# Kernel optimization log

Hardware: AMD Instinct MI355X
Metric: run time of the kernel (lower is better)

The kernel has to match this reference:

```python
import jax, jax.numpy as jnp
import numpy as np
import math

EPS = 1e-07
ITERATIONS = 3
FINAL_LAMBDA = 0.01

B, H, W, K, CIN, COUT, P = 8, 12, 12, 3, 16, 32, 16


def setup_inputs() -> dict:
    key = jax.random.key(0)
    k1, k2, k3, k4 = jax.random.split(key, 4)
    V = jax.random.normal(k1, (B, H, W, K, K, CIN, COUT, P), dtype=jnp.float32)
    a = jax.random.uniform(k2, (B, H, W, K, K, CIN, 1), dtype=jnp.float32)
    Beta_u = jax.random.normal(k3, (1, 1, 1, 1, 1, 1, COUT, 1), dtype=jnp.float32)
    Beta_a = jax.random.normal(k4, (1, 1, 1, 1, 1, 1, COUT), dtype=jnp.float32)
    R = jnp.full((B, H, W, K, K, CIN, COUT), 1.0 / COUT, dtype=jnp.float32)
    outSize = (B, H, W, COUT, P)
    return {"V": V, "a": a, "Beta_u": Beta_u, "Beta_a": Beta_a, "R": R, "outSize": outSize}


def _l2_normalize(x, axis):
    n = jnp.sqrt(jnp.sum(x * x, axis=axis, keepdims=True))
    return x / jnp.maximum(n, 1e-12)  # matches F.normalize default eps


def reference(V, a, Beta_u, Beta_a, R, outSize):
    mathpilog = jnp.log(jnp.asarray(2.0 * math.pi, dtype=jnp.float32))
    mu = sigma_sqr = a_out = None
    for i in range(ITERATIONS):
        Lam = FINAL_LAMBDA * (1.0 - 0.95 ** (i + 1))
        Rw = (R * a)[..., None]                                  # [B,h,w,K,K,Cin,Cout,1]
        mu_denom = jnp.sum(Rw, axis=(3, 4, 5), keepdims=True)    # [B,h,w,1,1,1,Cout,1]
        mu = jnp.sum(Rw * V, axis=(3, 4, 5), keepdims=True) / (mu_denom + EPS)  # [B,h,w,1,1,1,Cout,P]
        V_mu_sqr = (V - mu) ** 2                                 # [B,h,w,K,K,Cin,Cout,P]
        sigma_sqr = jnp.sum(Rw * V_mu_sqr, axis=(3, 4, 5), keepdims=True) / (mu_denom + EPS)
        cost_h = (Beta_u + 0.5 * jnp.log(sigma_sqr)) * mu_denom  # [B,h,w,1,1,1,Cout,P]
        x = Lam * (Beta_a - jnp.sum(cost_h, axis=7))             # [B,h,w,1,1,1,Cout]
        a_out = jax.nn.sigmoid(_l2_normalize(x, axis=6))
        log_p1 = -0.5 * jnp.sum(mathpilog + jnp.log(sigma_sqr), axis=7) + EPS
        log_p2 = -jnp.sum(V_mu_sqr / (2.0 * sigma_sqr + EPS), axis=7)  # [B,h,w,K,K,Cin,Cout]
        R = jax.nn.softmax(jnp.log(a_out) + log_p1 + log_p2, axis=6)
    mu_out = jnp.squeeze(mu).reshape(outSize)
    sigma_out = jnp.squeeze(sigma_sqr).reshape(outSize)
    return mu_out, jnp.squeeze(a_out), sigma_out
```

## Files before the change

kernel.cpp:

```cpp
#include <hip/hip_runtime.h>
#include <math.h>

#define NPOS 1152
#define NN   144
#define COUT 32
#define PP   16
#define EPSF 1e-7f
#define LOG2PI 1.8378770664093453f

#define MU_OFF   0
#define A_OFF    589824
#define SIG_OFF  626688

template<int CTRL>
__device__ __forceinline__ float dppf(float x) {
    return __int_as_float(__builtin_amdgcn_update_dpp(
        0, __float_as_int(x), CTRL, 0xf, 0xf, true));
}

__device__ __forceinline__ float redmax32(float m) {
    m = fmaxf(m, dppf<0xB1>(m));
    m = fmaxf(m, dppf<0x4E>(m));
    m = fmaxf(m, dppf<0x141>(m));
    m = fmaxf(m, dppf<0x140>(m));
    m = fmaxf(m, __shfl_xor(m, 16, 64));
    return m;
}
__device__ __forceinline__ float redsum32(float s) {
    s += dppf<0xB1>(s);
    s += dppf<0x4E>(s);
    s += dppf<0x141>(s);
    s += dppf<0x140>(s);
    s += __shfl_xor(s, 16, 64);
    return s;
}

__global__ void __launch_bounds__(256, 4)
em_routing_kernel(const float* __restrict__ V,
                  const float* __restrict__ a,
                  const float* __restrict__ Bu,
                  const float* __restrict__ Ba,
                  const float* __restrict__ Rin,
                  float* __restrict__ out)
{
    const int pos  = blockIdx.x;
    const int tid  = threadIdx.x;
    const int c    = tid & 31;
    const int slot = tid >> 5;
    const int wave = tid >> 6;

    const float* Vp = V + (size_t)pos * (NN * COUT * PP);
    const float* Rp = Rin + (size_t)pos * (NN * COUT);

    __shared__ float a_s[NN];
    __shared__ __align__(16) float red[2][4][32][36];

    for (int i = tid; i < NN; i += 256) a_s[i] = a[pos * NN + i];
    __syncthreads();

    const float Bu_c = Bu[c];
    const float Ba_c = Ba[c];

    float A_r[PP];
    float B2_r[PP];
    float cl2 = 0.f;
    float mu[PP], sg[PP];
    float ao = 0.f;

    #pragma unroll
    for (int it = 0; it < 3; ++it) {
        const float lam = 0.01f * (1.f - ((it == 0) ? 0.95f
                                         : (it == 1) ? 0.95f * 0.95f
                                                     : 0.95f * 0.95f * 0.95f));

        float S0 = 0.f, S1[PP], S2[PP];
        #pragma unroll
        for (int p = 0; p < PP; ++p) { S1[p] = 0.f; S2[p] = 0.f; }

        const float4* vq = (const float4*)(Vp + (size_t)slot * (COUT * PP) + c * PP);
        const float*  rq = Rp + slot * COUT + c;

        float4 n0 = vq[0], n1 = vq[1], n2 = vq[2], n3 = vq[3];
        float  rv = (it == 0) ? *rq : 0.f;

        #pragma unroll 1
        for (int j = 0; j < 18; ++j) {
            const float4 q0 = n0, q1 = n1, q2 = n2, q3 = n3;
            const float  rc = rv;
            if (j < 17) {
                vq += 1024;
                n0 = vq[0]; n1 = vq[1]; n2 = vq[2]; n3 = vq[3];
                if (it == 0) { rq += 256; rv = *rq; }
            }
            const float av = a_s[slot + (j << 3)];

            const float v[PP] = {q0.x,q0.y,q0.z,q0.w, q1.x,q1.y,q1.z,q1.w,
                                 q2.x,q2.y,q2.z,q2.w, q3.x,q3.y,q3.z,q3.w};
            float Rw;
            if (it == 0) {
                Rw = rc * av;
            } else {
                float logit = cl2;
                #pragma unroll
                for (int p = 0; p < PP; ++p) {
                    const float t = fmaf(-A_r[p], v[p], B2_r[p]);
                    logit = fmaf(t, v[p], logit);
                }
                const float m = redmax32(logit);
                const float e = __expf(logit - m);
                const float s = redsum32(e);
                Rw = __fdividef(e, s) * av;
            }
            S0 += Rw;
            #pragma unroll
            for (int p = 0; p < PP; ++p) {
                const float t = Rw * v[p];
                S1[p] += t;
                S2[p] = fmaf(t, v[p], S2[p]);
            }
        }

        S0 += __shfl_xor(S0, 32, 64);
        #pragma unroll
        for (int p = 0; p < PP; ++p) {
            S1[p] += __shfl_xor(S1[p], 32, 64);
            S2[p] += __shfl_xor(S2[p], 32, 64);
        }

        float* rb = &red[it & 1][wave][c][0];
        if ((tid & 32) == 0) {
            #pragma unroll
            for (int q = 0; q < 4; ++q)
                ((float4*)rb)[q] = make_float4(S1[4*q], S1[4*q+1], S1[4*q+2], S1[4*q+3]);
            rb[32] = S0;
        } else {
            #pragma unroll
            for (int q = 0; q < 4; ++q)
                ((float4*)rb)[4 + q] = make_float4(S2[4*q], S2[4*q+1], S2[4*q+2], S2[4*q+3]);
        }
        __syncthreads();

        float s1[PP], s2[PP], d0 = 0.f;
        #pragma unroll
        for (int p = 0; p < PP; ++p) { s1[p] = 0.f; s2[p] = 0.f; }
        #pragma unroll
        for (int w = 0; w < 4; ++w) {
            const float* rr = &red[it & 1][w][c][0];
            #pragma unroll
            for (int q = 0; q < 4; ++q) {
                const float4 x = ((const float4*)rr)[q];
                s1[4*q] += x.x; s1[4*q+1] += x.y; s1[4*q+2] += x.z; s1[4*q+3] += x.w;
            }
            #pragma unroll
            for (int q = 0; q < 4; ++q) {
                const float4 x = ((const float4*)rr)[4 + q];
                s2[4*q] += x.x; s2[4*q+1] += x.y; s2[4*q+2] += x.z; s2[4*q+3] += x.w;
            }
            d0 += rr[32];
        }

        const float inv = __fdividef(1.f, d0 + EPSF);
        float sumlog = 0.f;
        #pragma unroll
        for (int p = 0; p < PP; ++p) {
            const float m_ = s1[p] * inv;
            float g = (s2[p] - 2.f * m_ * s1[p] + m_ * m_ * d0) * inv;
            g = fmaxf(g, 1e-30f);
            mu[p] = m_;
            sg[p] = g;
            sumlog += __logf(g);
        }
        const float xs  = lam * (Ba_c - d0 * (16.f * Bu_c + 0.5f * sumlog));
        const float nn2 = redsum32(xs * xs);
        const float y   = xs / fmaxf(sqrtf(nn2), 1e-12f);
        ao = 1.f / (1.f + __expf(-y));
        const float cl = __logf(ao) - 0.5f * (16.f * LOG2PI + sumlog) + EPSF;

        float Cacc = 0.f;
        #pragma unroll
        for (int p = 0; p < PP; ++p) {
            const float wp = __fdividef(1.f, 2.f * sg[p] + EPSF);
            A_r[p]  = wp;
            B2_r[p] = 2.f * wp * mu[p];
            Cacc = fmaf(wp * mu[p], mu[p], Cacc);
        }
        cl2 = cl - Cacc;
    }

    if (tid < 32) {
        float4* mo = (float4*)(out + MU_OFF  + (size_t)pos * (COUT * PP) + c * PP);
        float4* so = (float4*)(out + SIG_OFF + (size_t)pos * (COUT * PP) + c * PP);
        #pragma unroll
        for (int q = 0; q < 4; ++q) {
            mo[q] = make_float4(mu[4*q], mu[4*q+1], mu[4*q+2], mu[4*q+3]);
            so[q] = make_float4(sg[4*q], sg[4*q+1], sg[4*q+2], sg[4*q+3]);
        }
        out[A_OFF + pos * COUT + c] = ao;
    }
}

extern "C" void kernel_launch(void* const* d_in, const int* in_sizes, int n_in,
                              void* d_out, int out_size, void* d_ws, size_t ws_size,
                              hipStream_t stream) {
    const float* V  = (const float*)d_in[0];
    const float* a  = (const float*)d_in[1];
    const float* Bu = (const float*)d_in[2];
    const float* Ba = (const float*)d_in[3];
    const float* R  = (const float*)d_in[4];
    float* out = (float*)d_out;
    em_routing_kernel<<<NPOS, 256, 0, stream>>>(V, a, Bu, Ba, R, out);
}
```

Measured before the change: 558.7 us.

## Deepen V prefetch to an 8-deep register ring and prefetch across iterations

Replaces the single-stage V prefetch with an 8-entry register ring buffer (and a matching one for R in the first iteration), fully unrolls the 18-step loop, and issues the next routing iteration's first loads before the reduction and barrier. The goal is to hide global memory latency for the streaming V reads, which are re-read three times. The first iteration is peeled so it skips the softmax path, and the loop bound is relaxed to 2 blocks per SM to make room for the larger register footprint. The added registers lower occupancy and could cause spills.

```diff
diff --git a/kernel.cpp b/kernel.cpp
--- a/kernel.cpp
+++ b/kernel.cpp
@@ -35,7 +35,101 @@
     return s;
 }
 
-__global__ void __launch_bounds__(256, 4)
+__device__ __forceinline__ void fold_write(float S0, float (&S1)[PP], float (&S2)[PP],
+                                           float (*rbw)[36], int tid, int c)
+{
+    S0 += __shfl_xor(S0, 32, 64);
+    #pragma unroll
+    for (int p = 0; p < PP; ++p) {
+        S1[p] += __shfl_xor(S1[p], 32, 64);
+        S2[p] += __shfl_xor(S2[p], 32, 64);
+    }
+    float* rb = rbw[c];
+    if ((tid & 32) == 0) {
+        #pragma unroll
+        for (int q = 0; q < 4; ++q)
+            ((float4*)rb)[q] = make_float4(S1[4*q], S1[4*q+1], S1[4*q+2], S1[4*q+3]);
+        rb[32] = S0;
+    } else {
+        #pragma unroll
+        for (int q = 0; q < 4; ++q)
+            ((float4*)rb)[4 + q] = make_float4(S2[4*q], S2[4*q+1], S2[4*q+2], S2[4*q+3]);
+    }
+}
+
+__device__ __forceinline__ void finalize_iter(
+    const float (&rb)[4][32][36], int c, int tid, int pos, float lam,
+    float Bu_c, float Ba_c, bool last,
+    float (&A_r)[PP], float (&B2_r)[PP], float& cl2, float* __restrict__ out)
+{
+    float s1[PP], s2[PP], d0 = 0.f;
+    #pragma unroll
+    for (int p = 0; p < PP; ++p) { s1[p] = 0.f; s2[p] = 0.f; }
+    #pragma unroll
+    for (int w = 0; w < 4; ++w) {
+        const float* rr = &rb[w][c][0];
+        #pragma unroll
+        for (int q = 0; q < 4; ++q) {
+            const float4 x = ((const float4*)rr)[q];
+            s1[4*q] += x.x; s1[4*q+1] += x.y; s1[4*q+2] += x.z; s1[4*q+3] += x.w;
+        }
+        #pragma unroll
+        for (int q = 0; q < 4; ++q) {
+            const float4 x = ((const float4*)rr)[4 + q];
+            s2[4*q] += x.x; s2[4*q+1] += x.y; s2[4*q+2] += x.z; s2[4*q+3] += x.w;
+        }
+        d0 += rr[32];
+    }
+
+    const float inv = __fdividef(1.f, d0 + EPSF);
+    float mu[PP], sg[PP], sumlog = 0.f;
+    #pragma unroll
+    for (int p = 0; p < PP; ++p) {
+        const float m_ = s1[p] * inv;
+        float g = (s2[p] - 2.f * m_ * s1[p] + m_ * m_ * d0) * inv;
+        g = fmaxf(g, 1e-30f);
+        mu[p] = m_;
+        sg[p] = g;
+        sumlog += __logf(g);
+    }
+    const float xs  = lam * (Ba_c - d0 * (16.f * Bu_c + 0.5f * sumlog));
+    const float nn2 = redsum32(xs * xs);
+    const float y   = xs / fmaxf(sqrtf(nn2), 1e-12f);
+    const float ao  = 1.f / (1.f + __expf(-y));
+
+    if (!last) {
+        const float cl = __logf(ao) - 0.5f * (16.f * LOG2PI + sumlog) + EPSF;
+        float Cacc = 0.f;
+        #pragma unroll
+        for (int p = 0; p < PP; ++p) {
+            const float wp = __fdividef(1.f, 2.f * sg[p] + EPSF);
+            A_r[p]  = wp;
+            B2_r[p] = 2.f * wp * mu[p];
+            Cacc = fmaf(wp * mu[p], mu[p], Cacc);
+        }
+        cl2 = cl - Cacc;
+    } else if (tid < 32) {
+        float4* mo = (float4*)(out + MU_OFF  + (size_t)pos * (COUT * PP) + c * PP);
+        float4* so = (float4*)(out + SIG_OFF + (size_t)pos * (COUT * PP) + c * PP);
+        #pragma unroll
+        for (int q = 0; q < 4; ++q) {
+            mo[q] = make_float4(mu[4*q], mu[4*q+1], mu[4*q+2], mu[4*q+3]);
+            so[q] = make_float4(sg[4*q], sg[4*q+1], sg[4*q+2], sg[4*q+3]);
+        }
+        out[A_OFF + pos * COUT + c] = ao;
+    }
+}
+
+#define LOADV(jj, j) do { const float4* p_ = vq + (size_t)(j) * 1024; \
+    buf[jj][0] = p_[0]; buf[jj][1] = p_[1]; buf[jj][2] = p_[2]; buf[jj][3] = p_[3]; } while (0)
+
+#define EXTRACT(vv, jj) const float vv[PP] = { \
+    buf[jj][0].x, buf[jj][0].y, buf[jj][0].z, buf[jj][0].w, \
+    buf[jj][1].x, buf[jj][1].y, buf[jj][1].z, buf[jj][1].w, \
+    buf[jj][2].x, buf[jj][2].y, buf[jj][2].z, buf[jj][2].w, \
+    buf[jj][3].x, buf[jj][3].y, buf[jj][3].z, buf[jj][3].w }
+
+__global__ void __launch_bounds__(256, 2)
 em_routing_kernel(const float* __restrict__ V,
                   const float* __restrict__ a,
                   const float* __restrict__ Bu,
@@ -61,56 +155,34 @@
     const float Bu_c = Bu[c];
     const float Ba_c = Ba[c];
 
-    float A_r[PP];
-    float B2_r[PP];
+    const float4* vq = (const float4*)(Vp + slot * (COUT * PP) + c * PP);
+    const float*  rq = Rp + slot * COUT + c;
+
+    float A_r[PP], B2_r[PP];
     float cl2 = 0.f;
-    float mu[PP], sg[PP];
-    float ao = 0.f;
-
-    #pragma unroll
-    for (int it = 0; it < 3; ++it) {
-        const float lam = 0.01f * (1.f - ((it == 0) ? 0.95f
-                                         : (it == 1) ? 0.95f * 0.95f
-                                                     : 0.95f * 0.95f * 0.95f));
-
+
+    float4 buf[8][4];
+
+    const float L0 = 0.01f * (1.f - 0.95f);
+    const float L1 = 0.01f * (1.f - 0.95f * 0.95f);
+    const float L2 = 0.01f * (1.f - 0.95f * 0.95f * 0.95f);
+
+    {
         float S0 = 0.f, S1[PP], S2[PP];
         #pragma unroll
         for (int p = 0; p < PP; ++p) { S1[p] = 0.f; S2[p] = 0.f; }
 
-        const float4* vq = (const float4*)(Vp + (size_t)slot * (COUT * PP) + c * PP);
-        const float*  rq = Rp + slot * COUT + c;
-
-        float4 n0 = vq[0], n1 = vq[1], n2 = vq[2], n3 = vq[3];
-        float  rv = (it == 0) ? *rq : 0.f;
-
-        #pragma unroll 1
+        float rbuf[8];
+        #pragma unroll
+        for (int jj = 0; jj < 8; ++jj) { LOADV(jj, jj); rbuf[jj] = rq[jj * 256]; }
+
+        #pragma unroll
         for (int j = 0; j < 18; ++j) {
-            const float4 q0 = n0, q1 = n1, q2 = n2, q3 = n3;
-            const float  rc = rv;
-            if (j < 17) {
-                vq += 1024;
-                n0 = vq[0]; n1 = vq[1]; n2 = vq[2]; n3 = vq[3];
-                if (it == 0) { rq += 256; rv = *rq; }
-            }
+            EXTRACT(v, j & 7);
+            const float rc = rbuf[j & 7];
+            if (j < 10) { LOADV(j & 7, j + 8); rbuf[j & 7] = rq[(j + 8) * 256]; }
             const float av = a_s[slot + (j << 3)];
-
-            const float v[PP] = {q0.x,q0.y,q0.z,q0.w, q1.x,q1.y,q1.z,q1.w,
-                                 q2.x,q2.y,q2.z,q2.w, q3.x,q3.y,q3.z,q3.w};
-            float Rw;
-            if (it == 0) {
-                Rw = rc * av;
-            } else {
-                float logit = cl2;
-                #pragma unroll
-                for (int p = 0; p < PP; ++p) {
-                    const float t = fmaf(-A_r[p], v[p], B2_r[p]);
-                    logit = fmaf(t, v[p], logit);
-                }
-                const float m = redmax32(logit);
-                const float e = __expf(logit - m);
-                const float s = redsum32(e);
-                Rw = __fdividef(e, s) * av;
-            }
+            const float Rw = rc * av;
             S0 += Rw;
             #pragma unroll
             for (int p = 0; p < PP; ++p) {
@@ -119,83 +191,52 @@
                 S2[p] = fmaf(t, v[p], S2[p]);
             }
         }
-
-        S0 += __shfl_xor(S0, 32, 64);
-        #pragma unroll
-        for (int p = 0; p < PP; ++p) {
-            S1[p] += __shfl_xor(S1[p], 32, 64);
-            S2[p] += __shfl_xor(S2[p], 32, 64);
-        }
-
-        float* rb = &red[it & 1][wave][c][0];
-        if ((tid & 32) == 0) {
-            #pragma unroll
-            for (int q = 0; q < 4; ++q)
-                ((float4*)rb)[q] = make_float4(S1[4*q], S1[4*q+1], S1[4*q+2], S1[4*q+3]);
-            rb[32] = S0;
-        } else {
-            #pragma unroll
-            for (int q = 0; q < 4; ++q)
-                ((float4*)rb)[4 + q] = make_float4(S2[4*q], S2[4*q+1], S2[4*q+2], S2[4*q+3]);
-        }
+        #pragma unroll
+        for (int jj = 0; jj < 8; ++jj) LOADV(jj, jj);
+
+        fold_write(S0, S1, S2, red[0][wave], tid, c);
         __syncthreads();
-
-        float s1[PP], s2[PP], d0 = 0.f;
-        #pragma unroll
-        for (int p = 0; p < PP; ++p) { s1[p] = 0.f; s2[p] = 0.f; }
-        #pragma unroll
-        for (int w = 0; w < 4; ++w) {
-            const float* rr = &red[it & 1][w][c][0];
-            #pragma unroll
-            for (int q = 0; q < 4; ++q) {
-                const float4 x = ((const float4*)rr)[q];
-                s1[4*q] += x.x; s1[4*q+1] += x.y; s1[4*q+2] += x.z; s1[4*q+3] += x.w;
+        finalize_iter(red[0], c, tid, pos, L0, Bu_c, Ba_c, false, A_r, B2_r, cl2, out);
+    }
+
+    #pragma unroll 1
+    for (int it = 1; it < 3; ++it) {
+        float S0 = 0.f, S1[PP], S2[PP];
+        #pragma unroll
+        for (int p = 0; p < PP; ++p) { S1[p] = 0.f; S2[p] = 0.f; }
+
+        #pragma unroll
+        for (int j = 0; j < 18; ++j) {
+            EXTRACT(v, j & 7);
+            if (j < 10) LOADV(j & 7, j + 8);
+            const float av = a_s[slot + (j << 3)];
+            float logit = cl2;
+            #pragma unroll
+            for (int p = 0; p < PP; ++p) {
+                const float t = fmaf(-A_r[p], v[p], B2_r[p]);
+                logit = fmaf(t, v[p], logit);
             }
-            #pragma unroll
-            for (int q = 0; q < 4; ++q) {
-                const float4 x = ((const float4*)rr)[4 + q];
-                s2[4*q] += x.x; s2[4*q+1] += x.y; s2[4*q+2] += x.z; s2[4*q+3] += x.w;
+            const float m = redmax32(logit);
+            const float e = __expf(logit - m);
+            const float s = redsum32(e);
+            const float Rw = __fdividef(e, s) * av;
+            S0 += Rw;
+            #pragma unroll
+            for (int p = 0; p < PP; ++p) {
+                const float t = Rw * v[p];
+                S1[p] += t;
+                S2[p] = fmaf(t, v[p], S2[p]);
             }
-            d0 += rr[32];
-        }
-
-        const float inv = __fdividef(1.f, d0 + EPSF);
-        float sumlog = 0.f;
-        #pragma unroll
-        for (int p = 0; p < PP; ++p) {
-            const float m_ = s1[p] * inv;
-            float g = (s2[p] - 2.f * m_ * s1[p] + m_ * m_ * d0) * inv;
-            g = fmaxf(g, 1e-30f);
-            mu[p] = m_;
-            sg[p] = g;
-            sumlog += __logf(g);
-        }
-        const float xs  = lam * (Ba_c - d0 * (16.f * Bu_c + 0.5f * sumlog));
-        const float nn2 = redsum32(xs * xs);
-        const float y   = xs / fmaxf(sqrtf(nn2), 1e-12f);
-        ao = 1.f / (1.f + __expf(-y));
-        const float cl = __logf(ao) - 0.5f * (16.f * LOG2PI + sumlog) + EPSF;
-
-        float Cacc = 0.f;
-        #pragma unroll
-        for (int p = 0; p < PP; ++p) {
-            const float wp = __fdividef(1.f, 2.f * sg[p] + EPSF);
-            A_r[p]  = wp;
-            B2_r[p] = 2.f * wp * mu[p];
-            Cacc = fmaf(wp * mu[p], mu[p], Cacc);
-        }
-        cl2 = cl - Cacc;
-    }
-
-    if (tid < 32) {
-        float4* mo = (float4*)(out + MU_OFF  + (size_t)pos * (COUT * PP) + c * PP);
-        float4* so = (float4*)(out + SIG_OFF + (size_t)pos * (COUT * PP) + c * PP);
-        #pragma unroll
-        for (int q = 0; q < 4; ++q) {
-            mo[q] = make_float4(mu[4*q], mu[4*q+1], mu[4*q+2], mu[4*q+3]);
-            so[q] = make_float4(sg[4*q], sg[4*q+1], sg[4*q+2], sg[4*q+3]);
-        }
-        out[A_OFF + pos * COUT + c] = ao;
+        }
+        if (it < 2) {
+            #pragma unroll
+            for (int jj = 0; jj < 8; ++jj) LOADV(jj, jj);
+        }
+
+        fold_write(S0, S1, S2, red[it & 1][wave], tid, c);
+        __syncthreads();
+        finalize_iter(red[it & 1], c, tid, pos, (it == 1) ? L1 : L2,
+                      Bu_c, Ba_c, (it == 2), A_r, B2_r, cl2, out);
     }
 }
 
```

Result: slower. 931.2 us (+66.7%).
